# Kernel tuning notes

Measured on AMD Instinct MI355X. Metric: run time of the kernel, lower is better.

The kernel has to match this reference:

```python
import jax, jax.numpy as jnp
import numpy as np

BS, N, H, W = 32, 8, 512, 512

def setup_inputs() -> dict:
    key = jax.random.key(0)
    k1, k2, k3 = jax.random.split(key, 3)
    pred_iou = jax.random.uniform(k1, (BS, N), dtype=jnp.float32)
    target_masks = jax.random.randint(k2, (BS, H, W), 0, 2, dtype=jnp.int32)
    pred_masks = jax.random.uniform(k3, (BS, N, H, W), dtype=jnp.float32)
    return {"pred_iou": pred_iou, "target_masks": target_masks, "pred_masks": pred_masks}

def reference(pred_iou, target_masks, pred_masks):
    # Binary Jaccard (torchmetrics): threshold preds at 0.5, target > 0.
    pred_bin = pred_masks > 0.5                      # [bs, n, H, W]
    tgt_bin = (target_masks > 0)[:, None, :, :]      # [bs, 1, H, W] broadcast over n
    inter = jnp.sum(pred_bin & tgt_bin, axis=(-2, -1)).astype(jnp.float32)  # [bs, n]
    union = jnp.sum(pred_bin | tgt_bin, axis=(-2, -1)).astype(jnp.float32)  # [bs, n]
    actual_iou = jnp.where(union > 0, inter / jnp.maximum(union, 1.0), 0.0)  # [bs, n]
    squared_error = (pred_iou - actual_iou) ** 2
    return squared_error
```

## Files before the change

### kernel.cpp

```cpp
#include <hip/hip_runtime.h>


#define BS      32
#define NMASKS  8
#define HW      (512 * 512)
#define GROUPS  8
#define SPAN    (HW / GROUPS)
#define BLOCK   256
#define NPAIRS  (BS * NMASKS)
#define PER_THREAD (SPAN / (BLOCK * 4))

typedef int   iv4 __attribute__((ext_vector_type(4)));
typedef float fv4 __attribute__((ext_vector_type(4)));

__global__ __launch_bounds__(BLOCK, 8) void iou_count_kernel(
    const int* __restrict__ tgt,
    const float* __restrict__ pred,
    unsigned long long* __restrict__ ws)
{
    const int idx = blockIdx.x;
    const int b   = idx >> 6;
    const int n   = (idx >> 3) & 7;
    const int grp = idx & 7;
    const int tid = threadIdx.x;

    const size_t tgt_base  = (size_t)b * HW + (size_t)grp * SPAN;
    const size_t pred_base = ((size_t)b * NMASKS + n) * HW + (size_t)grp * SPAN;

    unsigned int inter = 0u, uni = 0u;

#pragma unroll 4
    for (int it = 0; it < PER_THREAD; ++it) {
        const size_t off = (size_t)it * (BLOCK * 4) + (size_t)tid * 4;

        const iv4 t4 = *(const iv4*)(tgt + tgt_base + off);
        const fv4 p4 = __builtin_nontemporal_load(
            (const fv4*)(pred + pred_base + off));

        const int tb0 = t4.x > 0, tb1 = t4.y > 0, tb2 = t4.z > 0, tb3 = t4.w > 0;
        const int pb0 = p4.x > 0.5f, pb1 = p4.y > 0.5f,
                  pb2 = p4.z > 0.5f, pb3 = p4.w > 0.5f;

        inter += (unsigned)((pb0 & tb0) + (pb1 & tb1) + (pb2 & tb2) + (pb3 & tb3));
        uni   += (unsigned)((pb0 | tb0) + (pb1 | tb1) + (pb2 | tb2) + (pb3 | tb3));
    }

    unsigned long long v =
        ((unsigned long long)inter << 32) | (unsigned long long)uni;

    const int lane = tid & 63;
    const int wave = tid >> 6;
    __shared__ unsigned long long s[BLOCK / 64];

#pragma unroll
    for (int off = 32; off > 0; off >>= 1)
        v += __shfl_down(v, off);
    if (lane == 0) s[wave] = v;
    __syncthreads();

    if (tid == 0)
        ws[(size_t)grp * NPAIRS + (size_t)b * NMASKS + n] =
            s[0] + s[1] + s[2] + s[3];
}

__global__ __launch_bounds__(NPAIRS) void finalize_kernel(
    const float* __restrict__ pred_iou,
    const unsigned long long* __restrict__ ws,
    float* __restrict__ out)
{
    const int i = threadIdx.x;
    unsigned long long v = 0ull;
#pragma unroll
    for (int g = 0; g < GROUPS; ++g)
        v += ws[(size_t)g * NPAIRS + i];

    const unsigned int inter = (unsigned int)(v >> 32);
    const unsigned int uni   = (unsigned int)(v & 0xffffffffu);
    const float iou = (uni > 0u) ? ((float)inter / (float)uni) : 0.0f;
    const float d = pred_iou[i] - iou;
    out[i] = d * d;
}

extern "C" void kernel_launch(void* const* d_in, const int* in_sizes, int n_in,
                              void* d_out, int out_size, void* d_ws, size_t ws_size,
                              hipStream_t stream) {
    const float* pred_iou = (const float*)d_in[0];
    const int*   tgt      = (const int*)d_in[1];
    const float* pred     = (const float*)d_in[2];
    float* out = (float*)d_out;
    unsigned long long* ws = (unsigned long long*)d_ws;

    iou_count_kernel<<<BS * NMASKS * GROUPS, BLOCK, 0, stream>>>(tgt, pred, ws);
    finalize_kernel<<<1, NPAIRS, 0, stream>>>(pred_iou, ws, out);
}
```

Measured before the change: 368.7 us.

## Pack target mask into ballot bitmask and count IoU via popcount

Adds a pre-pass kernel that compresses the int32 target mask into 64-bit ballot words once per image, instead of re-reading the full target for each of the eight predicted masks. The count kernel then ballots the thresholded predictions and uses popcount with the bitmask to get wave-level intersection and union counts. This removes the per-lane shuffle reduction. It cuts redundant target memory traffic and per-element ALU work, at the cost of an extra kernel launch and a dependency on matching bit layouts.

```diff
diff --git a/kernel.cpp b/kernel.cpp
--- a/kernel.cpp
+++ b/kernel.cpp
@@ -4,18 +4,44 @@
 #define BS      32
 #define NMASKS  8
 #define HW      (512 * 512)
+#define WPI     (HW / 256)
+#define TOTAL_W (BS * WPI)
 #define GROUPS  8
 #define SPAN    (HW / GROUPS)
 #define BLOCK   256
 #define NPAIRS  (BS * NMASKS)
-#define PER_THREAD (SPAN / (BLOCK * 4))
+#define ITERS   (SPAN / (BLOCK * 4))
 
 typedef int   iv4 __attribute__((ext_vector_type(4)));
 typedef float fv4 __attribute__((ext_vector_type(4)));
 
+__global__ __launch_bounds__(BLOCK) void build_bitmask(
+    const int* __restrict__ tgt,
+    unsigned long long* __restrict__ bm)
+{
+    const int lane  = threadIdx.x & 63;
+    const int gwave = blockIdx.x * (BLOCK / 64) + (threadIdx.x >> 6);
+    const int w0    = gwave * (TOTAL_W / 1024);
+
+#pragma unroll 4
+    for (int i = 0; i < TOTAL_W / 1024; ++i) {
+        const int w = w0 + i;
+        const iv4 t4 = __builtin_nontemporal_load(
+            (const iv4*)(tgt + (size_t)w * 256 + (size_t)lane * 4));
+        const unsigned long long b0 = __ballot(t4.x > 0);
+        const unsigned long long b1 = __ballot(t4.y > 0);
+        const unsigned long long b2 = __ballot(t4.z > 0);
+        const unsigned long long b3 = __ballot(t4.w > 0);
+        if (lane == 0) {
+            unsigned long long* p = bm + (size_t)w * 4;
+            p[0] = b0; p[1] = b1; p[2] = b2; p[3] = b3;
+        }
+    }
+}
+
 __global__ __launch_bounds__(BLOCK, 8) void iou_count_kernel(
-    const int* __restrict__ tgt,
     const float* __restrict__ pred,
+    const unsigned long long* __restrict__ bm,
     unsigned long long* __restrict__ ws)
 {
     const int idx = blockIdx.x;
@@ -23,39 +49,38 @@
     const int n   = (idx >> 3) & 7;
     const int grp = idx & 7;
     const int tid = threadIdx.x;
+    const int wv  = tid >> 6;
 
-    const size_t tgt_base  = (size_t)b * HW + (size_t)grp * SPAN;
-    const size_t pred_base = ((size_t)b * NMASKS + n) * HW + (size_t)grp * SPAN;
+    const float* pbase =
+        pred + ((size_t)(b * NMASKS + n)) * HW + (size_t)grp * SPAN + (size_t)tid * 4;
+
+    const int wbase = __builtin_amdgcn_readfirstlane(
+        b * WPI + grp * (SPAN / 256) + wv);
 
     unsigned int inter = 0u, uni = 0u;
 
 #pragma unroll 4
-    for (int it = 0; it < PER_THREAD; ++it) {
-        const size_t off = (size_t)it * (BLOCK * 4) + (size_t)tid * 4;
+    for (int it = 0; it < ITERS; ++it) {
+        const fv4 p4 = __builtin_nontemporal_load(
+            (const fv4*)(pbase + (size_t)it * (BLOCK * 4)));
 
-        const iv4 t4 = *(const iv4*)(tgt + tgt_base + off);
-        const fv4 p4 = __builtin_nontemporal_load(
-            (const fv4*)(pred + pred_base + off));
+        const unsigned long long* wp = bm + (size_t)(wbase + it * 4) * 4;
+        const unsigned long long w0 = wp[0], w1 = wp[1], w2 = wp[2], w3 = wp[3];
 
-        const int tb0 = t4.x > 0, tb1 = t4.y > 0, tb2 = t4.z > 0, tb3 = t4.w > 0;
-        const int pb0 = p4.x > 0.5f, pb1 = p4.y > 0.5f,
-                  pb2 = p4.z > 0.5f, pb3 = p4.w > 0.5f;
+        const unsigned long long p0 = __ballot(p4.x > 0.5f);
+        const unsigned long long p1 = __ballot(p4.y > 0.5f);
+        const unsigned long long p2 = __ballot(p4.z > 0.5f);
+        const unsigned long long p3 = __ballot(p4.w > 0.5f);
 
-        inter += (unsigned)((pb0 & tb0) + (pb1 & tb1) + (pb2 & tb2) + (pb3 & tb3));
-        uni   += (unsigned)((pb0 | tb0) + (pb1 | tb1) + (pb2 | tb2) + (pb3 | tb3));
+        inter += (unsigned)(__popcll(p0 & w0) + __popcll(p1 & w1) +
+                            __popcll(p2 & w2) + __popcll(p3 & w3));
+        uni   += (unsigned)(__popcll(p0 | w0) + __popcll(p1 | w1) +
+                            __popcll(p2 | w2) + __popcll(p3 | w3));
     }
 
-    unsigned long long v =
-        ((unsigned long long)inter << 32) | (unsigned long long)uni;
-
-    const int lane = tid & 63;
-    const int wave = tid >> 6;
     __shared__ unsigned long long s[BLOCK / 64];
-
-#pragma unroll
-    for (int off = 32; off > 0; off >>= 1)
-        v += __shfl_down(v, off);
-    if (lane == 0) s[wave] = v;
+    if ((tid & 63) == 0)
+        s[wv] = ((unsigned long long)inter << 32) | (unsigned long long)uni;
     __syncthreads();
 
     if (tid == 0)
@@ -88,8 +113,11 @@
     const int*   tgt      = (const int*)d_in[1];
     const float* pred     = (const float*)d_in[2];
     float* out = (float*)d_out;
-    unsigned long long* ws = (unsigned long long*)d_ws;
 
-    iou_count_kernel<<<BS * NMASKS * GROUPS, BLOCK, 0, stream>>>(tgt, pred, ws);
-    finalize_kernel<<<1, NPAIRS, 0, stream>>>(pred_iou, ws, out);
+    unsigned long long* partials = (unsigned long long*)d_ws;
+    unsigned long long* bm = (unsigned long long*)((char*)d_ws + (64 << 10));
+
+    build_bitmask<<<1024 / (BLOCK / 64), BLOCK, 0, stream>>>(tgt, bm);
+    iou_count_kernel<<<BS * NMASKS * GROUPS, BLOCK, 0, stream>>>(pred, bm, partials);
+    finalize_kernel<<<1, NPAIRS, 0, stream>>>(pred_iou, partials, out);
 }
```

Measured after the change: 367.3 us. Within noise of the previous version (-0.4%).
